# Optimization experiments

Hardware: AMD Instinct MI355X
Metric: run time of the kernel (lower is better)

Reference implementation:

```python
import jax, jax.numpy as jnp
import numpy as np

N_NODES = 100000
N_EDGES = 1600000
N_FEAT = 128
HIDDEN = 64
N_CLASSES = 40


def setup_inputs() -> dict:
    key = jax.random.key(0)
    ks = jax.random.split(key, 4)
    x = jax.random.normal(ks[0], (N_NODES, N_FEAT), dtype=jnp.float32)
    edge_index = jax.random.randint(ks[1], (2, N_EDGES), 0, N_NODES, dtype=jnp.int64)
    # Glorot-style init like PyG GCNConv
    W1 = jax.random.normal(ks[2], (N_FEAT, HIDDEN), dtype=jnp.float32) * (1.0 / np.sqrt(N_FEAT))
    b1 = jnp.zeros((HIDDEN,), dtype=jnp.float32)
    W2 = jax.random.normal(ks[3], (HIDDEN, N_CLASSES), dtype=jnp.float32) * (1.0 / np.sqrt(HIDDEN))
    b2 = jnp.zeros((N_CLASSES,), dtype=jnp.float32)
    return {"x": x, "edge_index": edge_index, "W1": W1, "b1": b1, "W2": W2, "b2": b2}


def _gcn_conv(x, src, dst, norm, W, b, n_nodes):
    # PyG GCNConv: transform first, then normalized scatter-add aggregation
    h = x @ W                                   # [N, out]
    msg = h[src] * norm[:, None]                # [E+N, out] gather
    out = jax.ops.segment_sum(msg, dst, num_segments=n_nodes)  # scatter-add
    return out + b


def _norm_and_loops(edge_index, n_nodes):
    # add self-loops, symmetric normalization deg^{-1/2} A_hat deg^{-1/2}
    loop = jnp.arange(n_nodes, dtype=edge_index.dtype)
    src = jnp.concatenate([edge_index[0], loop])
    dst = jnp.concatenate([edge_index[1], loop])
    deg = jax.ops.segment_sum(jnp.ones_like(dst, dtype=jnp.float32), dst, num_segments=n_nodes)
    dinv = jnp.where(deg > 0, jax.lax.rsqrt(jnp.maximum(deg, 1.0)), 0.0)
    norm = dinv[src] * dinv[dst]
    return src, dst, norm


def reference(x, edge_index, W1, b1, W2, b2):
    n_nodes = x.shape[0]
    src, dst, norm = _norm_and_loops(edge_index, n_nodes)
    h = _gcn_conv(x, src, dst, norm, W1, b1, n_nodes)
    h = jax.nn.relu(h)
    h = _gcn_conv(h, src, dst, norm, W2, b2, n_nodes)
    return jax.nn.log_softmax(h, axis=1)
```

## Files before the change

kernel.cpp:

```cpp
#include <hip/hip_runtime.h>
#include <hip/hip_bf16.h>
#include <string.h>

#define N_FEAT 128
#define HIDDEN 64
#define N_CLS  40
#define FILL_BLOCKS 1024
#define CHUNK_EDGES 16384
#define STAGE_CAP 6144
#define B_BITS 6
#define SRC_BITS 17

typedef __bf16 bf16x8 __attribute__((ext_vector_type(8)));
typedef float  f32x4  __attribute__((ext_vector_type(4)));

union Frag { unsigned u[4]; bf16x8 v; };

static __device__ inline int get_xcc() {
    return (int)(__builtin_amdgcn_s_getreg((3 << 11) | 20) & 7u);
}


static __device__ inline unsigned pack_bf16(float a, float b) {
    unsigned ba = __float_as_uint(a);
    unsigned bb = __float_as_uint(b);
    unsigned ra = (ba + 0x7fffu + ((ba >> 16) & 1u)) >> 16;
    unsigned rb = (bb + 0x7fffu + ((bb >> 16) & 1u)) >> 16;
    return (ra & 0xffffu) | (rb << 16);
}

static __device__ inline float2 unpack_bf16(unsigned v) {
    return make_float2(__uint_as_float(v << 16), __uint_as_float(v & 0xffff0000u));
}


__global__ void detect_layout_kernel(const int* __restrict__ ei, int* __restrict__ flag) {
    int lane = threadIdx.x;
    int v = ei[2 * lane + 1];
    unsigned long long b = __ballot(v != 0);
    if (lane == 0) flag[0] = (b == 0ull) ? 1 : 0;
}


__global__ __launch_bounds__(256) void bucket_hist_kernel(const int* __restrict__ ei,
                                                          const int* __restrict__ flag,
                                                          unsigned* __restrict__ bcnt,
                                                          int E, int nbuk) {
    __shared__ unsigned h[2048];
    for (int i = threadIdx.x; i < nbuk; i += 256) h[i] = 0u;
    __syncthreads();
    bool is64 = (flag[0] != 0);
    if (is64) {
        int idx = blockIdx.x * 256 + threadIdx.x;
        int stride2 = gridDim.x * 256 * 2;
        int Eeven = E & ~1;
        for (int e = idx * 2; e < Eeven; e += stride2) {
            uint4 dv = *(const uint4*)(ei + (size_t)2 * E + (size_t)2 * e);
            atomicAdd(&h[((int)dv.x) >> B_BITS], 1u);
            atomicAdd(&h[((int)dv.z) >> B_BITS], 1u);
        }
        for (int e = Eeven + idx; e < E; e += gridDim.x * 256) {
            int d = ei[(size_t)2 * E + (size_t)2 * e];
            atomicAdd(&h[d >> B_BITS], 1u);
        }
    } else {
        const int* dstp = ei + E;
        for (int e = blockIdx.x * 256 + threadIdx.x; e < E; e += gridDim.x * 256) {
            int d = dstp[e];
            atomicAdd(&h[d >> B_BITS], 1u);
        }
    }
    __syncthreads();
    for (int i = threadIdx.x; i < nbuk; i += 256)
        if (h[i]) atomicAdd(&bcnt[i], h[i]);
}


__global__ __launch_bounds__(512) void bucket_scan_kernel(const unsigned* __restrict__ bcnt,
                                                          unsigned* __restrict__ bbase,
                                                          unsigned* __restrict__ bcur, int nbuk) {
    __shared__ unsigned tmp[512];
    __shared__ unsigned carry;
    if (threadIdx.x == 0) carry = 0u;
    __syncthreads();
    for (int base = 0; base < nbuk; base += 512) {
        int i = base + threadIdx.x;
        unsigned v = (i < nbuk) ? bcnt[i] : 0u;
        tmp[threadIdx.x] = v;
        __syncthreads();
#pragma unroll
        for (int off = 1; off < 512; off <<= 1) {
            unsigned t = (threadIdx.x >= (unsigned)off) ? tmp[threadIdx.x - off] : 0u;
            __syncthreads();
            tmp[threadIdx.x] += t;
            __syncthreads();
        }
        unsigned excl = tmp[threadIdx.x] - v + carry;
        if (i < nbuk) {
            bbase[i] = excl;
            bcur[(size_t)i * 16] = excl;
        }
        __syncthreads();
        if (threadIdx.x == 511) carry += tmp[511];
        __syncthreads();
    }
}


__global__ __launch_bounds__(256) void fill_buckets_kernel(const int* __restrict__ ei,
                                                           const int* __restrict__ flag,
                                                           unsigned* __restrict__ bcur,
                                                           unsigned* __restrict__ ctr,
                                                           unsigned* __restrict__ tmpbuf,
                                                           int E, int nbuk) {
    int r = get_xcc();
    int bpx = (nbuk + 7) >> 3;
    int blo = r * bpx;
    int bhi = min(nbuk, blo + bpx);
    int nlb = bhi - blo;
    bool is64 = (flag[0] != 0);
    const size_t dstoff = (size_t)2 * E;

    __shared__ unsigned stage[STAGE_CAP];
    __shared__ unsigned hist[256], lbase[256], lcur[256];
    __shared__ unsigned tail_s, chunk_s;

    int lane = threadIdx.x & 63;
    unsigned long long lmask_lt = (lane == 0) ? 0ull : ((~0ull) >> (64 - lane));

    auto stage_edge = [&](bool own, unsigned v, unsigned lb) {
        unsigned long long mask = __ballot(own ? 1 : 0);
        int cnt = __popcll(mask);
        if (cnt) {
            unsigned bp = 0;
            int leader = __builtin_ctzll(mask);
            if (lane == leader) bp = atomicAdd(&tail_s, (unsigned)cnt);
            bp = __shfl(bp, leader);
            if (own) {
                unsigned pos = bp + (unsigned)__popcll(mask & lmask_lt);
                if (pos < STAGE_CAP) {
                    stage[pos] = v;
                    atomicAdd(&hist[lb], 1u);
                } else {
                    unsigned slot = __hip_atomic_fetch_add(&bcur[(size_t)(blo + (int)lb) * 16], 1u,
                                                           __ATOMIC_RELAXED, __HIP_MEMORY_SCOPE_WORKGROUP);
                    tmpbuf[slot] = v & 0x7fffffu;
                }
            }
        }
    };

    for (;;) {
        if (threadIdx.x == 0) {
            chunk_s = __hip_atomic_fetch_add(&ctr[r * 64], 1u, __ATOMIC_RELAXED,
                                             __HIP_MEMORY_SCOPE_WORKGROUP);
            tail_s = 0u;
        }
        if (threadIdx.x < 256) { hist[threadIdx.x] = 0u; lcur[threadIdx.x] = 0u; }
        __syncthreads();
        long long base = (long long)chunk_s * CHUNK_EDGES;
        if (base >= E) break;
        int end = (int)min((long long)E, base + CHUNK_EDGES);

        if (is64) {
            for (int e = (int)base + 2 * threadIdx.x; e + 1 < end; e += 512) {
                uint4 sv = *(const uint4*)(ei + (size_t)2 * e);
                uint4 dv = *(const uint4*)(ei + dstoff + (size_t)2 * e);
                {
                    int d = (int)dv.x;
                    int b = d >> B_BITS;
                    bool own = (b >= blo && b < bhi);
                    unsigned lb = own ? (unsigned)(b - blo) : 0u;
                    unsigned v = (lb << 23) | ((unsigned)(d & ((1 << B_BITS) - 1)) << SRC_BITS) | sv.x;
                    stage_edge(own, v, lb);
                }
                {
                    int d = (int)dv.z;
                    int b = d >> B_BITS;
                    bool own = (b >= blo && b < bhi);
                    unsigned lb = own ? (unsigned)(b - blo) : 0u;
                    unsigned v = (lb << 23) | ((unsigned)(d & ((1 << B_BITS) - 1)) << SRC_BITS) | sv.z;
                    stage_edge(own, v, lb);
                }
            }
            if ((end - (int)base) & 1) {
                bool own = false; unsigned v = 0, lb = 0;
                if (threadIdx.x == 0) {
                    int e = end - 1;
                    int d = ei[dstoff + (size_t)2 * e];
                    int b = d >> B_BITS;
                    if (b >= blo && b < bhi) {
                        own = true; lb = (unsigned)(b - blo);
                        v = (lb << 23) | ((unsigned)(d & ((1 << B_BITS) - 1)) << SRC_BITS)
                            | (unsigned)ei[(size_t)2 * e];
                    }
                }
                stage_edge(own, v, lb);
            }
        } else {
            for (int e = (int)base + threadIdx.x; e < end; e += 256) {
                int d = ei[(size_t)E + e];
                int b = d >> B_BITS;
                bool own = (b >= blo && b < bhi);
                unsigned lb = own ? (unsigned)(b - blo) : 0u;
                unsigned v = (lb << 23) | ((unsigned)(d & ((1 << B_BITS) - 1)) << SRC_BITS)
                             | (own ? (unsigned)ei[e] : 0u);
                stage_edge(own, v, lb);
            }
        }
        __syncthreads();

        for (int lb = threadIdx.x; lb < nlb; lb += 256) {
            unsigned h = hist[lb];
            if (h) lbase[lb] = __hip_atomic_fetch_add(&bcur[(size_t)(blo + lb) * 16], h,
                                                      __ATOMIC_RELAXED, __HIP_MEMORY_SCOPE_WORKGROUP);
        }
        __syncthreads();

        unsigned tl = min(tail_s, (unsigned)STAGE_CAP);
        for (unsigned i = threadIdx.x; i < tl; i += 256) {
            unsigned v = stage[i];
            unsigned lb = v >> 23;
            unsigned off = atomicAdd(&lcur[lb], 1u);
            tmpbuf[lbase[lb] + off] = v & 0x7fffffu;
        }
        __syncthreads();
    }
}


__global__ __launch_bounds__(256) void bucket_to_csr_kernel(const unsigned* __restrict__ tmpbuf,
                                                            const unsigned* __restrict__ bbase,
                                                            unsigned* __restrict__ deg,
                                                            unsigned* __restrict__ rowptr,
                                                            float* __restrict__ dinv,
                                                            int* __restrict__ csr_src,
                                                            int nbuk, int N, int E) {
    int b = blockIdx.x;
    int tid = threadIdx.x;
    unsigned beg = bbase[b];
    unsigned end = (b + 1 < nbuk) ? bbase[b + 1] : (unsigned)E;
    int d0 = b << B_BITS;
    const int ND = 1 << B_BITS;
    __shared__ unsigned hist[ND], scn[ND], cur[ND];
    if (tid < ND) { hist[tid] = 0u; cur[tid] = 0u; }
    __syncthreads();
    for (unsigned i = beg + tid; i < end; i += 256)
        atomicAdd(&hist[tmpbuf[i] >> SRC_BITS], 1u);
    __syncthreads();
    if (tid == 0) {
        unsigned run = 0;
        for (int k = 0; k < ND; ++k) { scn[k] = run; run += hist[k]; }
    }
    __syncthreads();
    if (tid < ND) {
        int d = d0 + tid;
        if (d < N) {
            unsigned dg = hist[tid];
            deg[d] = dg;
            dinv[d] = rsqrtf((float)(dg + 1u));
            rowptr[d] = beg + scn[tid];
        }
    }
    __syncthreads();
    for (unsigned i = beg + tid; i < end; i += 256) {
        unsigned v = tmpbuf[i];
        unsigned dl = v >> SRC_BITS;
        unsigned s = v & ((1u << SRC_BITS) - 1u);
        unsigned p = atomicAdd(&cur[dl], 1u);
        csr_src[beg + scn[dl] + p] = (int)s;
    }
}


__global__ __launch_bounds__(256) void gemm1_mfma_kernel(const float* __restrict__ x,
                                                         const float* __restrict__ W1,
                                                         unsigned* __restrict__ h1b, int N) {
    int lane = threadIdx.x & 63;
    int quad = lane >> 4;
    int col  = lane & 15;

    Frag B[4][4];
#pragma unroll
    for (int c = 0; c < 4; ++c)
#pragma unroll
        for (int ks = 0; ks < 4; ++ks) {
            int n = c * 16 + col;
#pragma unroll
            for (int jj = 0; jj < 4; ++jj) {
                int k = ks * 32 + quad * 8 + 2 * jj;
                B[c][ks].u[jj] = pack_bf16(W1[k * HIDDEN + n], W1[(k + 1) * HIDDEN + n]);
            }
        }

    int wave_id = blockIdx.x * 4 + (threadIdx.x >> 6);
    int nwaves  = gridDim.x * 4;
    int ntiles  = (N + 15) >> 4;

    for (int rt = wave_id; rt < ntiles; rt += nwaves) {
        int rowA = rt * 16 + col;
        Frag A[4];
#pragma unroll
        for (int ks = 0; ks < 4; ++ks) {
            float4 a0 = make_float4(0.f, 0.f, 0.f, 0.f), a1 = a0;
            if (rowA < N) {
                const float4* ap = (const float4*)(x + (size_t)rowA * N_FEAT + ks * 32 + quad * 8);
                a0 = ap[0];
                a1 = ap[1];
            }
            A[ks].u[0] = pack_bf16(a0.x, a0.y);
            A[ks].u[1] = pack_bf16(a0.z, a0.w);
            A[ks].u[2] = pack_bf16(a1.x, a1.y);
            A[ks].u[3] = pack_bf16(a1.z, a1.w);
        }
        f32x4 acc[4] = {{0.f, 0.f, 0.f, 0.f}, {0.f, 0.f, 0.f, 0.f},
                        {0.f, 0.f, 0.f, 0.f}, {0.f, 0.f, 0.f, 0.f}};
#pragma unroll
        for (int ks = 0; ks < 4; ++ks)
#pragma unroll
            for (int c = 0; c < 4; ++c)
                acc[c] = __builtin_amdgcn_mfma_f32_16x16x32_bf16(A[ks].v, B[c][ks].v, acc[c], 0, 0, 0);

        int rowD = rt * 16 + quad * 4;
#pragma unroll
        for (int c = 0; c < 4; ++c)
#pragma unroll
            for (int r = 0; r < 4; ++r) {
                float v = acc[c][r];
                float nxt = __shfl_down(v, 1);
                int row = rowD + r;
                if (((lane & 1) == 0) && row < N)
                    h1b[(size_t)row * 32 + ((c * 16 + col) >> 1)] = pack_bf16(v, nxt);
            }
    }
}


__global__ __launch_bounds__(256) void gemm2_mfma_kernel(const unsigned* __restrict__ actb,
                                                         const float* __restrict__ W2,
                                                         unsigned* __restrict__ h2b, int N) {
    int lane = threadIdx.x & 63;
    int quad = lane >> 4;
    int col  = lane & 15;

    Frag B[3][2];
#pragma unroll
    for (int c = 0; c < 3; ++c)
#pragma unroll
        for (int ks = 0; ks < 2; ++ks) {
            int n = c * 16 + col;
#pragma unroll
            for (int jj = 0; jj < 4; ++jj) {
                int k = ks * 32 + quad * 8 + 2 * jj;
                float w0 = (n < N_CLS) ? W2[k * N_CLS + n] : 0.f;
                float w1 = (n < N_CLS) ? W2[(k + 1) * N_CLS + n] : 0.f;
                B[c][ks].u[jj] = pack_bf16(w0, w1);
            }
        }

    int wave_id = blockIdx.x * 4 + (threadIdx.x >> 6);
    int nwaves  = gridDim.x * 4;
    int ntiles  = (N + 15) >> 4;

    for (int rt = wave_id; rt < ntiles; rt += nwaves) {
        int rowA = rt * 16 + col;
        Frag A[2];
#pragma unroll
        for (int ks = 0; ks < 2; ++ks) {
            uint4 u = make_uint4(0u, 0u, 0u, 0u);
            if (rowA < N)
                u = *(const uint4*)(actb + (size_t)rowA * 32 + ks * 16 + quad * 4);
            A[ks].u[0] = u.x; A[ks].u[1] = u.y; A[ks].u[2] = u.z; A[ks].u[3] = u.w;
        }
        f32x4 acc[3] = {{0.f, 0.f, 0.f, 0.f}, {0.f, 0.f, 0.f, 0.f}, {0.f, 0.f, 0.f, 0.f}};
#pragma unroll
        for (int ks = 0; ks < 2; ++ks)
#pragma unroll
            for (int c = 0; c < 3; ++c)
                acc[c] = __builtin_amdgcn_mfma_f32_16x16x32_bf16(A[ks].v, B[c][ks].v, acc[c], 0, 0, 0);

        int rowD = rt * 16 + quad * 4;
#pragma unroll
        for (int c = 0; c < 3; ++c)
#pragma unroll
            for (int r = 0; r < 4; ++r) {
                float v = acc[c][r];
                float nxt = __shfl_down(v, 1);
                int row = rowD + r;
                int pair = (c * 16 + col) >> 1;
                if (((lane & 1) == 0) && pair < 20 && row < N)
                    h2b[(size_t)row * 20 + pair] = pack_bf16(v, nxt);
            }
    }
}


__global__ __launch_bounds__(256) void agg1_kernel(const unsigned* __restrict__ h1b,
                                                   const int* __restrict__ csr_src,
                                                   const unsigned* __restrict__ rowptr,
                                                   const unsigned* __restrict__ deg,
                                                   const float* __restrict__ dinv,
                                                   const float* __restrict__ b1,
                                                   unsigned* __restrict__ actb, int N) {
    int wave = threadIdx.x >> 6, lane = threadIdx.x & 63;
    int sub = lane >> 5, j = lane & 31;
    int d = blockIdx.x * 4 + wave;
    if (d >= N) return;
    float dv = dinv[d];
    float acc0 = 0.f, acc1 = 0.f;
    if (sub == 0) {
        float2 v = unpack_bf16(h1b[(size_t)d * 32 + j]);
        acc0 = dv * v.x; acc1 = dv * v.y;
    }
    unsigned beg = rowptr[d];
    int len = (int)deg[d];
    int i = 0;
    for (; i + 8 <= len; i += 8) {
        int s0 = csr_src[beg + i + sub];
        int s1 = csr_src[beg + i + 2 + sub];
        int s2 = csr_src[beg + i + 4 + sub];
        int s3 = csr_src[beg + i + 6 + sub];
        float w0 = dinv[s0], w1 = dinv[s1], w2 = dinv[s2], w3 = dinv[s3];
        unsigned v0 = h1b[(size_t)s0 * 32 + j];
        unsigned v1 = h1b[(size_t)s1 * 32 + j];
        unsigned v2 = h1b[(size_t)s2 * 32 + j];
        unsigned v3 = h1b[(size_t)s3 * 32 + j];
        float2 a0 = unpack_bf16(v0), a1 = unpack_bf16(v1);
        float2 a2 = unpack_bf16(v2), a3 = unpack_bf16(v3);
        acc0 += w0 * a0.x + w1 * a1.x + w2 * a2.x + w3 * a3.x;
        acc1 += w0 * a0.y + w1 * a1.y + w2 * a2.y + w3 * a3.y;
    }
    for (; i + 4 <= len; i += 4) {
        int sA = csr_src[beg + i + sub];
        int sB = csr_src[beg + i + 2 + sub];
        float wA = dinv[sA], wB = dinv[sB];
        float2 a = unpack_bf16(h1b[(size_t)sA * 32 + j]);
        float2 b = unpack_bf16(h1b[(size_t)sB * 32 + j]);
        acc0 += wA * a.x + wB * b.x;
        acc1 += wA * a.y + wB * b.y;
    }
    for (; i < len; i += 2) {
        int e = i + sub;
        if (e < len) {
            int s = csr_src[beg + e];
            float w = dinv[s];
            float2 a = unpack_bf16(h1b[(size_t)s * 32 + j]);
            acc0 += w * a.x;
            acc1 += w * a.y;
        }
    }
    acc0 += __shfl_xor(acc0, 32);
    acc1 += __shfl_xor(acc1, 32);
    if (sub == 0) {
        float2 bb = ((const float2*)b1)[j];
        float r0 = fmaxf(acc0 * dv + bb.x, 0.f);
        float r1 = fmaxf(acc1 * dv + bb.y, 0.f);
        actb[(size_t)d * 32 + j] = pack_bf16(r0, r1);
    }
}


__global__ __launch_bounds__(256) void agg2_lsm_kernel(const unsigned* __restrict__ h2b,
                                                       const int* __restrict__ csr_src,
                                                       const unsigned* __restrict__ rowptr,
                                                       const unsigned* __restrict__ deg,
                                                       const float* __restrict__ dinv,
                                                       const float* __restrict__ b2,
                                                       float* __restrict__ out, int N) {
    int wave = threadIdx.x >> 6, lane = threadIdx.x & 63;
    int sub = lane >> 5, j = lane & 31;
    bool act = (j < 20);
    int d = blockIdx.x * 4 + wave;
    if (d >= N) return;
    float dv = dinv[d];
    float acc0 = 0.f, acc1 = 0.f;
    if (sub == 0 && act) {
        float2 v = unpack_bf16(h2b[(size_t)d * 20 + j]);
        acc0 = dv * v.x; acc1 = dv * v.y;
    }
    unsigned beg = rowptr[d];
    int len = (int)deg[d];
    int i = 0;
    for (; i + 8 <= len; i += 8) {
        int s0 = csr_src[beg + i + sub];
        int s1 = csr_src[beg + i + 2 + sub];
        int s2 = csr_src[beg + i + 4 + sub];
        int s3 = csr_src[beg + i + 6 + sub];
        float w0 = dinv[s0], w1 = dinv[s1], w2 = dinv[s2], w3 = dinv[s3];
        if (act) {
            float2 a0 = unpack_bf16(h2b[(size_t)s0 * 20 + j]);
            float2 a1 = unpack_bf16(h2b[(size_t)s1 * 20 + j]);
            float2 a2 = unpack_bf16(h2b[(size_t)s2 * 20 + j]);
            float2 a3 = unpack_bf16(h2b[(size_t)s3 * 20 + j]);
            acc0 += w0 * a0.x + w1 * a1.x + w2 * a2.x + w3 * a3.x;
            acc1 += w0 * a0.y + w1 * a1.y + w2 * a2.y + w3 * a3.y;
        }
    }
    for (; i + 4 <= len; i += 4) {
        int sA = csr_src[beg + i + sub];
        int sB = csr_src[beg + i + 2 + sub];
        float wA = dinv[sA], wB = dinv[sB];
        if (act) {
            float2 a = unpack_bf16(h2b[(size_t)sA * 20 + j]);
            float2 b = unpack_bf16(h2b[(size_t)sB * 20 + j]);
            acc0 += wA * a.x + wB * b.x;
            acc1 += wA * a.y + wB * b.y;
        }
    }
    for (; i < len; i += 2) {
        int e = i + sub;
        if (e < len && act) {
            int s = csr_src[beg + e];
            float w = dinv[s];
            float2 a = unpack_bf16(h2b[(size_t)s * 20 + j]);
            acc0 += w * a.x;
            acc1 += w * a.y;
        }
    }
    acc0 += __shfl_xor(acc0, 32);
    acc1 += __shfl_xor(acc1, 32);
    float v0 = -1e30f, v1 = -1e30f;
    if (act) {
        float2 bb = ((const float2*)b2)[j];
        v0 = acc0 * dv + bb.x;
        v1 = acc1 * dv + bb.y;
    }
    float m = fmaxf(v0, v1);
#pragma unroll
    for (int off = 32; off > 0; off >>= 1)
        m = fmaxf(m, __shfl_xor(m, off));
    float ex = (act && sub == 0) ? (expf(v0 - m) + expf(v1 - m)) : 0.f;
#pragma unroll
    for (int off = 32; off > 0; off >>= 1)
        ex += __shfl_xor(ex, off);
    float ls = logf(ex);
    if (act && sub == 0) {
        float2* orow = (float2*)(out + (size_t)d * N_CLS);
        orow[j] = make_float2(v0 - m - ls, v1 - m - ls);
    }
}


static inline size_t align_up(size_t x) { return (x + 255) & ~(size_t)255; }

extern "C" void kernel_launch(void* const* d_in, const int* in_sizes, int n_in,
                              void* d_out, int out_size, void* d_ws, size_t ws_size,
                              hipStream_t stream) {
    const float* x  = (const float*)d_in[0];
    const int*   ei = (const int*)d_in[1];
    const float* W1 = (const float*)d_in[2];
    const float* b1 = (const float*)d_in[3];
    const float* W2 = (const float*)d_in[4];
    const float* b2 = (const float*)d_in[5];

    int N = in_sizes[0] / N_FEAT;
    int E = in_sizes[1] / 2;
    int nbuk = (N + (1 << B_BITS) - 1) >> B_BITS;

    char* ws = (char*)d_ws;
    int*      flag    = (int*)ws;       ws += 256;
    unsigned* ctrs    = (unsigned*)ws;  ws += 4096;
    unsigned* bcnt    = (unsigned*)ws;  ws += align_up((size_t)nbuk * 4);
    unsigned* bbase   = (unsigned*)ws;  ws += align_up((size_t)nbuk * 4);
    unsigned* bcur    = (unsigned*)ws;  ws += align_up((size_t)nbuk * 64);
    unsigned* deg     = (unsigned*)ws;  ws += align_up((size_t)N * 4);
    float*    dinv    = (float*)ws;     ws += align_up((size_t)N * 4);
    unsigned* rowptr  = (unsigned*)ws;  ws += align_up((size_t)N * 4);
    unsigned* tmpbuf  = (unsigned*)ws;  ws += align_up((size_t)E * 4);
    int*      csr_src = (int*)ws;       ws += align_up((size_t)E * 4);
    unsigned* h1b     = (unsigned*)ws;  ws += align_up((size_t)N * 32 * 4);
    unsigned* actb    = (unsigned*)ws;  ws += align_up((size_t)N * 32 * 4);
    unsigned* h2b     = (unsigned*)ws;  ws += align_up((size_t)N * 20 * 4);

    hipMemsetAsync(ctrs, 0, 4096, stream);
    hipMemsetAsync(bcnt, 0, (size_t)nbuk * 4, stream);

    detect_layout_kernel<<<1, 64, 0, stream>>>(ei, flag);
    bucket_hist_kernel<<<256, 256, 0, stream>>>(ei, flag, bcnt, E, nbuk);
    bucket_scan_kernel<<<1, 512, 0, stream>>>(bcnt, bbase, bcur, nbuk);
    fill_buckets_kernel<<<FILL_BLOCKS, 256, 0, stream>>>(ei, flag, bcur, ctrs, tmpbuf, E, nbuk);
    bucket_to_csr_kernel<<<nbuk, 256, 0, stream>>>(tmpbuf, bbase, deg, rowptr, dinv, csr_src, nbuk, N, E);

    gemm1_mfma_kernel<<<512, 256, 0, stream>>>(x, W1, h1b, N);
    agg1_kernel<<<(N + 3) / 4, 256, 0, stream>>>(h1b, csr_src, rowptr, deg, dinv, b1, actb, N);

    gemm2_mfma_kernel<<<512, 256, 0, stream>>>(actb, W2, h2b, N);
    agg2_lsm_kernel<<<(N + 3) / 4, 256, 0, stream>>>(h2b, csr_src, rowptr, deg, dinv, b2, (float*)d_out, N);
}
```

Measured before the change: 321.8 us.

## Shard hidden features per XCC and reorder layer-two to aggregate before GEMM

Result: slower. 779.4 us (+142.2%).

```diff
diff --git a/kernel.cpp b/kernel.cpp
--- a/kernel.cpp
+++ b/kernel.cpp
@@ -6,6 +6,7 @@
 #define HIDDEN 64
 #define N_CLS  40
 #define FILL_BLOCKS 1024
+#define AGG_BLOCKS 1024
 #define CHUNK_EDGES 16384
 #define STAGE_CAP 6144
 #define B_BITS 6
@@ -275,7 +276,7 @@
 
 __global__ __launch_bounds__(256) void gemm1_mfma_kernel(const float* __restrict__ x,
                                                          const float* __restrict__ W1,
-                                                         unsigned* __restrict__ h1b, int N) {
+                                                         unsigned* __restrict__ h1s, int N) {
     int lane = threadIdx.x & 63;
     int quad = lane >> 4;
     int col  = lane & 15;
@@ -329,214 +330,169 @@
                 float v = acc[c][r];
                 float nxt = __shfl_down(v, 1);
                 int row = rowD + r;
-                if (((lane & 1) == 0) && row < N)
-                    h1b[(size_t)row * 32 + ((c * 16 + col) >> 1)] = pack_bf16(v, nxt);
-            }
-    }
-}
-
-
-__global__ __launch_bounds__(256) void gemm2_mfma_kernel(const unsigned* __restrict__ actb,
-                                                         const float* __restrict__ W2,
-                                                         unsigned* __restrict__ h2b, int N) {
+                if (((lane & 1) == 0) && row < N) {
+                    int pair = (c * 16 + col) >> 1;
+                    int shard = pair >> 2, slot = pair & 3;
+                    h1s[(size_t)shard * N * 4 + (size_t)row * 4 + slot] = pack_bf16(v, nxt);
+                }
+            }
+    }
+}
+
+
+__global__ __launch_bounds__(256) void agg1s_kernel(const unsigned* __restrict__ h1s,
+                                                    const int* __restrict__ csr_src,
+                                                    const unsigned* __restrict__ rowptr,
+                                                    const unsigned* __restrict__ deg,
+                                                    const float* __restrict__ dinv,
+                                                    const float* __restrict__ b1,
+                                                    unsigned* __restrict__ acts,
+                                                    unsigned* __restrict__ ctr2, int N) {
+    int r = get_xcc();
+    const unsigned* tab = h1s + (size_t)r * N * 4;
+    unsigned* otab = acts + (size_t)r * N * 4;
     int lane = threadIdx.x & 63;
-    int quad = lane >> 4;
-    int col  = lane & 15;
-
-    Frag B[3][2];
-#pragma unroll
-    for (int c = 0; c < 3; ++c)
-#pragma unroll
-        for (int ks = 0; ks < 2; ++ks) {
-            int n = c * 16 + col;
-#pragma unroll
-            for (int jj = 0; jj < 4; ++jj) {
-                int k = ks * 32 + quad * 8 + 2 * jj;
-                float w0 = (n < N_CLS) ? W2[k * N_CLS + n] : 0.f;
-                float w1 = (n < N_CLS) ? W2[(k + 1) * N_CLS + n] : 0.f;
-                B[c][ks].u[jj] = pack_bf16(w0, w1);
-            }
-        }
-
-    int wave_id = blockIdx.x * 4 + (threadIdx.x >> 6);
-    int nwaves  = gridDim.x * 4;
-    int ntiles  = (N + 15) >> 4;
-
-    for (int rt = wave_id; rt < ntiles; rt += nwaves) {
-        int rowA = rt * 16 + col;
-        Frag A[2];
-#pragma unroll
-        for (int ks = 0; ks < 2; ++ks) {
-            uint4 u = make_uint4(0u, 0u, 0u, 0u);
-            if (rowA < N)
-                u = *(const uint4*)(actb + (size_t)rowA * 32 + ks * 16 + quad * 4);
-            A[ks].u[0] = u.x; A[ks].u[1] = u.y; A[ks].u[2] = u.z; A[ks].u[3] = u.w;
-        }
-        f32x4 acc[3] = {{0.f, 0.f, 0.f, 0.f}, {0.f, 0.f, 0.f, 0.f}, {0.f, 0.f, 0.f, 0.f}};
-#pragma unroll
-        for (int ks = 0; ks < 2; ++ks)
-#pragma unroll
-            for (int c = 0; c < 3; ++c)
-                acc[c] = __builtin_amdgcn_mfma_f32_16x16x32_bf16(A[ks].v, B[c][ks].v, acc[c], 0, 0, 0);
-
-        int rowD = rt * 16 + quad * 4;
-#pragma unroll
-        for (int c = 0; c < 3; ++c)
-#pragma unroll
-            for (int r = 0; r < 4; ++r) {
-                float v = acc[c][r];
-                float nxt = __shfl_down(v, 1);
-                int row = rowD + r;
-                int pair = (c * 16 + col) >> 1;
-                if (((lane & 1) == 0) && pair < 20 && row < N)
-                    h2b[(size_t)row * 20 + pair] = pack_bf16(v, nxt);
-            }
-    }
-}
-
-
-__global__ __launch_bounds__(256) void agg1_kernel(const unsigned* __restrict__ h1b,
-                                                   const int* __restrict__ csr_src,
-                                                   const unsigned* __restrict__ rowptr,
-                                                   const unsigned* __restrict__ deg,
-                                                   const float* __restrict__ dinv,
-                                                   const float* __restrict__ b1,
-                                                   unsigned* __restrict__ actb, int N) {
-    int wave = threadIdx.x >> 6, lane = threadIdx.x & 63;
-    int sub = lane >> 5, j = lane & 31;
-    int d = blockIdx.x * 4 + wave;
-    if (d >= N) return;
-    float dv = dinv[d];
-    float acc0 = 0.f, acc1 = 0.f;
-    if (sub == 0) {
-        float2 v = unpack_bf16(h1b[(size_t)d * 32 + j]);
-        acc0 = dv * v.x; acc1 = dv * v.y;
-    }
-    unsigned beg = rowptr[d];
-    int len = (int)deg[d];
-    int i = 0;
-    for (; i + 8 <= len; i += 8) {
-        int s0 = csr_src[beg + i + sub];
-        int s1 = csr_src[beg + i + 2 + sub];
-        int s2 = csr_src[beg + i + 4 + sub];
-        int s3 = csr_src[beg + i + 6 + sub];
-        float w0 = dinv[s0], w1 = dinv[s1], w2 = dinv[s2], w3 = dinv[s3];
-        unsigned v0 = h1b[(size_t)s0 * 32 + j];
-        unsigned v1 = h1b[(size_t)s1 * 32 + j];
-        unsigned v2 = h1b[(size_t)s2 * 32 + j];
-        unsigned v3 = h1b[(size_t)s3 * 32 + j];
-        float2 a0 = unpack_bf16(v0), a1 = unpack_bf16(v1);
-        float2 a2 = unpack_bf16(v2), a3 = unpack_bf16(v3);
-        acc0 += w0 * a0.x + w1 * a1.x + w2 * a2.x + w3 * a3.x;
-        acc1 += w0 * a0.y + w1 * a1.y + w2 * a2.y + w3 * a3.y;
-    }
-    for (; i + 4 <= len; i += 4) {
-        int sA = csr_src[beg + i + sub];
-        int sB = csr_src[beg + i + 2 + sub];
-        float wA = dinv[sA], wB = dinv[sB];
-        float2 a = unpack_bf16(h1b[(size_t)sA * 32 + j]);
-        float2 b = unpack_bf16(h1b[(size_t)sB * 32 + j]);
-        acc0 += wA * a.x + wB * b.x;
-        acc1 += wA * a.y + wB * b.y;
-    }
-    for (; i < len; i += 2) {
-        int e = i + sub;
-        if (e < len) {
-            int s = csr_src[beg + e];
-            float w = dinv[s];
-            float2 a = unpack_bf16(h1b[(size_t)s * 32 + j]);
-            acc0 += w * a.x;
-            acc1 += w * a.y;
-        }
-    }
-    acc0 += __shfl_xor(acc0, 32);
-    acc1 += __shfl_xor(acc1, 32);
-    if (sub == 0) {
-        float2 bb = ((const float2*)b1)[j];
-        float r0 = fmaxf(acc0 * dv + bb.x, 0.f);
-        float r1 = fmaxf(acc1 * dv + bb.y, 0.f);
-        actb[(size_t)d * 32 + j] = pack_bf16(r0, r1);
-    }
-}
-
-
-__global__ __launch_bounds__(256) void agg2_lsm_kernel(const unsigned* __restrict__ h2b,
-                                                       const int* __restrict__ csr_src,
-                                                       const unsigned* __restrict__ rowptr,
-                                                       const unsigned* __restrict__ deg,
-                                                       const float* __restrict__ dinv,
+    int wave = threadIdx.x >> 6;
+    int el = lane >> 2, slot = lane & 3;
+    float2 bb = ((const float2*)b1)[r * 4 + slot];
+    int nchunks = (N + 255) >> 8;
+    __shared__ unsigned chunk_s;
+    int k0 = (blockIdx.x >> 3) & 31;
+    for (int pass = 0; pass < 32; ++pass) {
+        int k = (k0 + pass) & 31;
+        unsigned* cp = &ctr2[(size_t)(r * 32 + k) * 16];
+        for (;;) {
+            if (threadIdx.x == 0) chunk_s = atomicAdd(cp, 1u);
+            __syncthreads();
+            unsigned idx = chunk_s;
+            __syncthreads();
+            unsigned chunk = (unsigned)k + 32u * idx;
+            if (chunk >= (unsigned)nchunks) break;
+            int d0 = (int)chunk * 256 + wave * 64;
+            int d1 = min(N, d0 + 64);
+            for (int d = d0; d < d1; ++d) {
+                unsigned beg = rowptr[d];
+                int len = (int)deg[d];
+                float dv = dinv[d];
+                float acc0 = 0.f, acc1 = 0.f;
+                if (el == 0) {
+                    float2 sv = unpack_bf16(tab[(size_t)d * 4 + slot]);
+                    acc0 = dv * sv.x; acc1 = dv * sv.y;
+                }
+                for (int i = el; i < len; i += 16) {
+                    int s = csr_src[beg + i];
+                    float w = dinv[s];
+                    float2 a = unpack_bf16(tab[(size_t)s * 4 + slot]);
+                    acc0 += w * a.x; acc1 += w * a.y;
+                }
+                acc0 += __shfl_xor(acc0, 4);  acc1 += __shfl_xor(acc1, 4);
+                acc0 += __shfl_xor(acc0, 8);  acc1 += __shfl_xor(acc1, 8);
+                acc0 += __shfl_xor(acc0, 16); acc1 += __shfl_xor(acc1, 16);
+                acc0 += __shfl_xor(acc0, 32); acc1 += __shfl_xor(acc1, 32);
+                if (el == 0) {
+                    float r0 = fmaxf(acc0 * dv + bb.x, 0.f);
+                    float r1 = fmaxf(acc1 * dv + bb.y, 0.f);
+                    otab[(size_t)d * 4 + slot] = pack_bf16(r0, r1);
+                }
+            }
+        }
+    }
+}
+
+
+__global__ __launch_bounds__(256) void agg2s_kernel(const unsigned* __restrict__ acts,
+                                                    const int* __restrict__ csr_src,
+                                                    const unsigned* __restrict__ rowptr,
+                                                    const unsigned* __restrict__ deg,
+                                                    const float* __restrict__ dinv,
+                                                    unsigned* __restrict__ gbs,
+                                                    unsigned* __restrict__ ctr2, int N) {
+    int r = get_xcc();
+    const unsigned* tab = acts + (size_t)r * N * 4;
+    unsigned* otab = gbs + (size_t)r * N * 4;
+    int lane = threadIdx.x & 63;
+    int wave = threadIdx.x >> 6;
+    int el = lane >> 2, slot = lane & 3;
+    int nchunks = (N + 255) >> 8;
+    __shared__ unsigned chunk_s;
+    int k0 = (blockIdx.x >> 3) & 31;
+    for (int pass = 0; pass < 32; ++pass) {
+        int k = (k0 + pass) & 31;
+        unsigned* cp = &ctr2[(size_t)(r * 32 + k) * 16];
+        for (;;) {
+            if (threadIdx.x == 0) chunk_s = atomicAdd(cp, 1u);
+            __syncthreads();
+            unsigned idx = chunk_s;
+            __syncthreads();
+            unsigned chunk = (unsigned)k + 32u * idx;
+            if (chunk >= (unsigned)nchunks) break;
+            int d0 = (int)chunk * 256 + wave * 64;
+            int d1 = min(N, d0 + 64);
+            for (int d = d0; d < d1; ++d) {
+                unsigned beg = rowptr[d];
+                int len = (int)deg[d];
+                float dv = dinv[d];
+                float acc0 = 0.f, acc1 = 0.f;
+                if (el == 0) {
+                    float2 sv = unpack_bf16(tab[(size_t)d * 4 + slot]);
+                    acc0 = dv * sv.x; acc1 = dv * sv.y;
+                }
+                for (int i = el; i < len; i += 16) {
+                    int s = csr_src[beg + i];
+                    float w = dinv[s];
+                    float2 a = unpack_bf16(tab[(size_t)s * 4 + slot]);
+                    acc0 += w * a.x; acc1 += w * a.y;
+                }
+                acc0 += __shfl_xor(acc0, 4);  acc1 += __shfl_xor(acc1, 4);
+                acc0 += __shfl_xor(acc0, 8);  acc1 += __shfl_xor(acc1, 8);
+                acc0 += __shfl_xor(acc0, 16); acc1 += __shfl_xor(acc1, 16);
+                acc0 += __shfl_xor(acc0, 32); acc1 += __shfl_xor(acc1, 32);
+                if (el == 0)
+                    otab[(size_t)d * 4 + slot] = pack_bf16(acc0 * dv, acc1 * dv);
+            }
+        }
+    }
+}
+
+
+__global__ __launch_bounds__(256) void gemm2lsm_kernel(const unsigned* __restrict__ gbs,
+                                                       const float* __restrict__ W2,
                                                        const float* __restrict__ b2,
                                                        float* __restrict__ out, int N) {
-    int wave = threadIdx.x >> 6, lane = threadIdx.x & 63;
-    int sub = lane >> 5, j = lane & 31;
-    bool act = (j < 20);
-    int d = blockIdx.x * 4 + wave;
+    int d = blockIdx.x * 256 + threadIdx.x;
     if (d >= N) return;
-    float dv = dinv[d];
-    float acc0 = 0.f, acc1 = 0.f;
-    if (sub == 0 && act) {
-        float2 v = unpack_bf16(h2b[(size_t)d * 20 + j]);
-        acc0 = dv * v.x; acc1 = dv * v.y;
-    }
-    unsigned beg = rowptr[d];
-    int len = (int)deg[d];
-    int i = 0;
-    for (; i + 8 <= len; i += 8) {
-        int s0 = csr_src[beg + i + sub];
-        int s1 = csr_src[beg + i + 2 + sub];
-        int s2 = csr_src[beg + i + 4 + sub];
-        int s3 = csr_src[beg + i + 6 + sub];
-        float w0 = dinv[s0], w1 = dinv[s1], w2 = dinv[s2], w3 = dinv[s3];
-        if (act) {
-            float2 a0 = unpack_bf16(h2b[(size_t)s0 * 20 + j]);
-            float2 a1 = unpack_bf16(h2b[(size_t)s1 * 20 + j]);
-            float2 a2 = unpack_bf16(h2b[(size_t)s2 * 20 + j]);
-            float2 a3 = unpack_bf16(h2b[(size_t)s3 * 20 + j]);
-            acc0 += w0 * a0.x + w1 * a1.x + w2 * a2.x + w3 * a3.x;
-            acc1 += w0 * a0.y + w1 * a1.y + w2 * a2.y + w3 * a3.y;
-        }
-    }
-    for (; i + 4 <= len; i += 4) {
-        int sA = csr_src[beg + i + sub];
-        int sB = csr_src[beg + i + 2 + sub];
-        float wA = dinv[sA], wB = dinv[sB];
-        if (act) {
-            float2 a = unpack_bf16(h2b[(size_t)sA * 20 + j]);
-            float2 b = unpack_bf16(h2b[(size_t)sB * 20 + j]);
-            acc0 += wA * a.x + wB * b.x;
-            acc1 += wA * a.y + wB * b.y;
-        }
-    }
-    for (; i < len; i += 2) {
-        int e = i + sub;
-        if (e < len && act) {
-            int s = csr_src[beg + e];
-            float w = dinv[s];
-            float2 a = unpack_bf16(h2b[(size_t)s * 20 + j]);
-            acc0 += w * a.x;
-            acc1 += w * a.y;
-        }
-    }
-    acc0 += __shfl_xor(acc0, 32);
-    acc1 += __shfl_xor(acc1, 32);
-    float v0 = -1e30f, v1 = -1e30f;
-    if (act) {
-        float2 bb = ((const float2*)b2)[j];
-        v0 = acc0 * dv + bb.x;
-        v1 = acc1 * dv + bb.y;
-    }
-    float m = fmaxf(v0, v1);
-#pragma unroll
-    for (int off = 32; off > 0; off >>= 1)
-        m = fmaxf(m, __shfl_xor(m, off));
-    float ex = (act && sub == 0) ? (expf(v0 - m) + expf(v1 - m)) : 0.f;
-#pragma unroll
-    for (int off = 32; off > 0; off >>= 1)
-        ex += __shfl_xor(ex, off);
-    float ls = logf(ex);
-    if (act && sub == 0) {
-        float2* orow = (float2*)(out + (size_t)d * N_CLS);
-        orow[j] = make_float2(v0 - m - ls, v1 - m - ls);
+    float z[N_CLS];
+#pragma unroll
+    for (int c = 0; c < N_CLS; ++c) z[c] = b2[c];
+
+#pragma unroll
+    for (int s = 0; s < 8; ++s) {
+        uint4 u = *(const uint4*)(gbs + (size_t)s * N * 4 + (size_t)d * 4);
+        float2 f0 = unpack_bf16(u.x), f1 = unpack_bf16(u.y);
+        float2 f2 = unpack_bf16(u.z), f3 = unpack_bf16(u.w);
+        float f[8] = {f0.x, f0.y, f1.x, f1.y, f2.x, f2.y, f3.x, f3.y};
+#pragma unroll
+        for (int q = 0; q < 8; ++q) {
+            int k = s * 8 + q;
+#pragma unroll
+            for (int c = 0; c < N_CLS; ++c)
+                z[c] = fmaf(f[q], W2[k * N_CLS + c], z[c]);
+        }
+    }
+    float m = z[0];
+#pragma unroll
+    for (int c = 1; c < N_CLS; ++c) m = fmaxf(m, z[c]);
+    float s = 0.f;
+#pragma unroll
+    for (int c = 0; c < N_CLS; ++c) s += __expf(z[c] - m);
+    float ls = __logf(s) + m;
+    float4* orow = (float4*)(out + (size_t)d * N_CLS);
+#pragma unroll
+    for (int q = 0; q < 10; ++q) {
+        float4 o;
+        o.x = z[q * 4 + 0] - ls; o.y = z[q * 4 + 1] - ls;
+        o.z = z[q * 4 + 2] - ls; o.w = z[q * 4 + 3] - ls;
+        orow[q] = o;
     }
 }
 
@@ -556,10 +512,13 @@
     int N = in_sizes[0] / N_FEAT;
     int E = in_sizes[1] / 2;
     int nbuk = (N + (1 << B_BITS) - 1) >> B_BITS;
+    int nblk = (N + 255) / 256;
 
     char* ws = (char*)d_ws;
     int*      flag    = (int*)ws;       ws += 256;
     unsigned* ctrs    = (unsigned*)ws;  ws += 4096;
+    unsigned* ctr2a   = (unsigned*)ws;  ws += 32768;
+    unsigned* ctr2b   = (unsigned*)ws;  ws += 32768;
     unsigned* bcnt    = (unsigned*)ws;  ws += align_up((size_t)nbuk * 4);
     unsigned* bbase   = (unsigned*)ws;  ws += align_up((size_t)nbuk * 4);
     unsigned* bcur    = (unsigned*)ws;  ws += align_up((size_t)nbuk * 64);
@@ -568,11 +527,11 @@
     unsigned* rowptr  = (unsigned*)ws;  ws += align_up((size_t)N * 4);
     unsigned* tmpbuf  = (unsigned*)ws;  ws += align_up((size_t)E * 4);
     int*      csr_src = (int*)ws;       ws += align_up((size_t)E * 4);
-    unsigned* h1b     = (unsigned*)ws;  ws += align_up((size_t)N * 32 * 4);
-    unsigned* actb    = (unsigned*)ws;  ws += align_up((size_t)N * 32 * 4);
-    unsigned* h2b     = (unsigned*)ws;  ws += align_up((size_t)N * 20 * 4);
-
-    hipMemsetAsync(ctrs, 0, 4096, stream);
+    unsigned* h1s     = (unsigned*)ws;  ws += align_up((size_t)N * 32 * 4);
+    unsigned* acts    = (unsigned*)ws;  ws += align_up((size_t)N * 32 * 4);
+    unsigned* gbs     = (unsigned*)ws;  ws += align_up((size_t)N * 32 * 4);
+
+    hipMemsetAsync(ctrs, 0, 4096 + 32768 + 32768, stream);
     hipMemsetAsync(bcnt, 0, (size_t)nbuk * 4, stream);
 
     detect_layout_kernel<<<1, 64, 0, stream>>>(ei, flag);
@@ -581,9 +540,9 @@
     fill_buckets_kernel<<<FILL_BLOCKS, 256, 0, stream>>>(ei, flag, bcur, ctrs, tmpbuf, E, nbuk);
     bucket_to_csr_kernel<<<nbuk, 256, 0, stream>>>(tmpbuf, bbase, deg, rowptr, dinv, csr_src, nbuk, N, E);
 
-    gemm1_mfma_kernel<<<512, 256, 0, stream>>>(x, W1, h1b, N);
-    agg1_kernel<<<(N + 3) / 4, 256, 0, stream>>>(h1b, csr_src, rowptr, deg, dinv, b1, actb, N);
-
-    gemm2_mfma_kernel<<<512, 256, 0, stream>>>(actb, W2, h2b, N);
-    agg2_lsm_kernel<<<(N + 3) / 4, 256, 0, stream>>>(h2b, csr_src, rowptr, deg, dinv, b2, (float*)d_out, N);
-}
+    gemm1_mfma_kernel<<<512, 256, 0, stream>>>(x, W1, h1s, N);
+    agg1s_kernel<<<AGG_BLOCKS, 256, 0, stream>>>(h1s, csr_src, rowptr, deg, dinv, b1, acts, ctr2a, N);
+
+    agg2s_kernel<<<AGG_BLOCKS, 256, 0, stream>>>(acts, csr_src, rowptr, deg, dinv, gbs, ctr2b, N);
+    gemm2lsm_kernel<<<nblk, 256, 0, stream>>>(gbs, W2, b2, (float*)d_out, N);
+}
```
